# Performance work log

Hardware: AMD Instinct MI355X
Metric: run time of the kernel (lower is better)

The kernel has to match this reference:

```python
import jax, jax.numpy as jnp
import numpy as np


def _sepconv1x1(x, dw, pw, b):
    # SeparableConv2D with kernel=1: depthwise 1x1 = per-channel scale, then pointwise matmul
    return jnp.einsum('nhwc,cd->nhwd', x * dw, pw) + b


def setup_inputs() -> dict:
    key = jax.random.key(0)
    ks = jax.random.split(key, 12)
    N, H, W, C_in, C_red = 4, 64, 64, 256, 64
    s = 0.05  # small init so softmax logits are well-conditioned
    return {
        'feature_maps': jax.random.normal(ks[0], (N, H, W, C_in), jnp.float32),
        'global_channel_output': jax.random.normal(ks[1], (N, H, W, C_in), jnp.float32),
        'dw_q': jax.random.normal(ks[2], (C_in,), jnp.float32) * s,
        'pw_q': jax.random.normal(ks[3], (C_in, C_red), jnp.float32) * s,
        'b_q': jnp.zeros((C_red,), jnp.float32),
        'dw_k': jax.random.normal(ks[4], (C_in,), jnp.float32) * s,
        'pw_k': jax.random.normal(ks[5], (C_in, C_red), jnp.float32) * s,
        'b_k': jnp.zeros((C_red,), jnp.float32),
        'dw_v': jax.random.normal(ks[6], (C_in,), jnp.float32) * s,
        'pw_v': jax.random.normal(ks[7], (C_in, C_red), jnp.float32) * s,
        'b_v': jnp.zeros((C_red,), jnp.float32),
        'dw_a': jax.random.normal(ks[8], (C_red,), jnp.float32) * s,
        'pw_a': jax.random.normal(ks[9], (C_red, C_in), jnp.float32) * s,
        'b_a': jnp.zeros((C_in,), jnp.float32),
    }


def reference(feature_maps, global_channel_output,
              dw_q, pw_q, b_q, dw_k, pw_k, b_k, dw_v, pw_v, b_v,
              dw_a, pw_a, b_a):
    N, H, W, _ = feature_maps.shape
    q = _sepconv1x1(feature_maps, dw_q, pw_q, b_q)  # [N,H,W,Cr]
    k = _sepconv1x1(feature_maps, dw_k, pw_k, b_k)
    v = _sepconv1x1(feature_maps, dw_v, pw_v, b_v)
    Cr = q.shape[-1]
    q = q.reshape(N, H * W, Cr)
    k = k.reshape(N, H * W, Cr)
    v = v.reshape(N, H * W, Cr)
    # tf.matmul(key, query, transpose_b=True): scores[i,j] = key_i . query_j
    scores = jnp.einsum('nic,njc->nij', k, q)  # [N,HW,HW]
    scores = jax.nn.softmax(scores, axis=-1)
    # tf.matmul(value, scores, transpose_a=True) -> [N,Cr,HW]
    att = jnp.einsum('nic,nij->ncj', v, scores)
    # faithful raw reshape (as in the original TF code) from [N,Cr,HW] to [N,H,W,Cr]
    att = att.reshape(N, H, W, Cr)
    att = _sepconv1x1(att, dw_a, pw_a, b_a)  # [N,H,W,C_in]
    return global_channel_output * att + global_channel_output
```

## Files before the change

kernel.cpp:

```cpp
#include <hip/hip_runtime.h>
#include <hip/hip_bf16.h>

typedef __attribute__((ext_vector_type(8))) __bf16 bf16x8;
typedef __attribute__((ext_vector_type(4))) float floatx4;
typedef __attribute__((ext_vector_type(4))) unsigned short us4;
typedef __attribute__((ext_vector_type(8))) unsigned short us8;
typedef __attribute__((ext_vector_type(4))) short s16x4;
typedef __attribute__((ext_vector_type(2))) unsigned int uint2v;

#define MFMA16(A, B, C) __builtin_amdgcn_mfma_f32_16x16x32_bf16((A), (B), (C), 0, 0, 0)
#define MFMA1K(A, B, C) __builtin_amdgcn_mfma_f32_16x16x16bf16_1k((A), (B), (C), 0, 0, 0)

static __device__ __forceinline__ unsigned short f2bfbits(float f) {
    __hip_bfloat16 h = __float2bfloat16(f);
    union { __hip_bfloat16 h; unsigned short u; } cv;
    cv.h = h;
    return cv.u;
}
static __device__ __forceinline__ unsigned int rne32(float f) {
    unsigned int u = __builtin_bit_cast(unsigned int, f);
    return u + 0x7fffu + ((u >> 16) & 1u);
}
static __device__ __forceinline__ unsigned short rne16(float f) {
    return (unsigned short)(rne32(f) >> 16);
}
static __device__ __forceinline__ s16x4 pack4(float e0, float e1, float e2, float e3) {
    unsigned int pa = __builtin_amdgcn_perm(rne32(e1), rne32(e0), 0x07060302u);
    unsigned int pb = __builtin_amdgcn_perm(rne32(e3), rne32(e2), 0x07060302u);
    uint2v u = {pa, pb};
    return __builtin_bit_cast(s16x4, u);
}
static __device__ __forceinline__ bf16x8 load_bf8(const __hip_bfloat16* p) {
    return *reinterpret_cast<const bf16x8*>(p);
}
static __device__ __forceinline__ bf16x8 cvt8(floatx4 a, floatx4 b) {
    us8 u;
#pragma unroll
    for (int i = 0; i < 4; i++) { u[i] = rne16(a[i]); u[4 + i] = rne16(b[i]); }
    return __builtin_bit_cast(bf16x8, u);
}
static __device__ __forceinline__ float bf2f(unsigned short u) {
    unsigned int w = ((unsigned int)u) << 16;
    return __builtin_bit_cast(float, w);
}


__global__ __launch_bounds__(256) void prep_w(
    const float* __restrict__ dwq, const float* __restrict__ pwq,
    const float* __restrict__ dwk, const float* __restrict__ pwk,
    const float* __restrict__ dwv, const float* __restrict__ pwv,
    __hip_bfloat16* __restrict__ wT)
{
    int idx = blockIdx.x * 256 + threadIdx.x;
    int p = idx >> 14;
    int r = idx & 16383;
    int d = r >> 8, c = r & 255;
    const float* dw = (p == 0) ? dwq : ((p == 1) ? dwk : dwv);
    const float* pw = (p == 0) ? pwq : ((p == 1) ? pwk : pwv);
    wT[idx] = __float2bfloat16(dw[c] * pw[c * 64 + d]);
}

__global__ __launch_bounds__(256) void proj_qkv(
    const float* __restrict__ x,
    const __hip_bfloat16* __restrict__ wT,
    const float* __restrict__ bqp, const float* __restrict__ bkp,
    const float* __restrict__ bvp,
    __hip_bfloat16* __restrict__ qf, __hip_bfloat16* __restrict__ kf,
    __hip_bfloat16* __restrict__ vf)
{
    int wg = blockIdx.x * 4 + (threadIdx.x >> 6);
    int p = wg >> 10;
    int wid = wg & 1023;
    int lane = threadIdx.x & 63;
    int l15 = lane & 15, quad = lane >> 4;
    int strip = wid << 4;

    floatx4 acc[4];
#pragma unroll
    for (int t = 0; t < 4; t++) acc[t] = (floatx4){0.f, 0.f, 0.f, 0.f};

    const float* xrow = x + (strip + l15) * 256 + quad * 8;
    const __hip_bfloat16* wp = wT + p * 16384;
#pragma unroll
    for (int ks = 0; ks < 8; ks++) {
        floatx4 xa = *reinterpret_cast<const floatx4*>(xrow + ks * 32);
        floatx4 xb = *reinterpret_cast<const floatx4*>(xrow + ks * 32 + 4);
        bf16x8 a = cvt8(xa, xb);
#pragma unroll
        for (int t = 0; t < 4; t++) {
            bf16x8 b = load_bf8(wp + (t * 16 + l15) * 256 + ks * 32 + quad * 8);
            acc[t] = MFMA16(a, b, acc[t]);
        }
    }
    if (p < 2) {
        __hip_bfloat16* dst = (p == 0) ? qf : kf;
        const float* bias = (p == 0) ? bqp : bkp;
#pragma unroll
        for (int t = 0; t < 4; t++) {
            float bsv = bias[t * 16 + l15];
            int off0 = wid * 1024 + (t >> 1) * 512 +
                       (((((t & 1) << 1) | (l15 >> 3)) * 16 + quad * 4) * 8) + (l15 & 7);
#pragma unroll
            for (int r = 0; r < 4; r++)
                dst[off0 + r * 8] = __float2bfloat16(acc[t][r] + bsv);
        }
    } else {
#pragma unroll
        for (int t = 0; t < 4; t++) {
            float bsv = bvp[t * 16 + l15];
            us4 pk;
#pragma unroll
            for (int r = 0; r < 4; r++) pk[r] = f2bfbits(acc[t][r] + bsv);
            *reinterpret_cast<us4*>(vf + (wid * 4 + t) * 256 + lane * 4) = pk;
        }
    }
}

__global__ __launch_bounds__(512) void pass1_rl(
    const __hip_bfloat16* __restrict__ qf, const __hip_bfloat16* __restrict__ kf,
    const __hip_bfloat16* __restrict__ vf, __hip_bfloat16* __restrict__ vfs)
{
    int itg0 = blockIdx.x * 2;
    int n = itg0 >> 8;
    int jw = threadIdx.x >> 6;
    int lane = threadIdx.x & 63;
    int l15 = lane & 15, quad = lane >> 4;

    const __hip_bfloat16* kp = kf + itg0 * 1024 + lane * 8;
    bf16x8 a0 = load_bf8(kp);
    bf16x8 a1 = load_bf8(kp + 512);
    bf16x8 a2 = load_bf8(kp + 1024);
    bf16x8 a3 = load_bf8(kp + 1536);

    floatx4 lsA = (floatx4){0.f, 0.f, 0.f, 0.f};
    floatx4 lsB = (floatx4){0.f, 0.f, 0.f, 0.f};
    const __hip_bfloat16* qp0 = qf + (n * 256 + jw * 32) * 1024 + lane * 8;
    for (int it = 0; it < 16; it++, qp0 += 2048) {
        bf16x8 b0 = load_bf8(qp0);
        bf16x8 b1 = load_bf8(qp0 + 512);
        bf16x8 b2 = load_bf8(qp0 + 1024);
        bf16x8 b3 = load_bf8(qp0 + 1536);
        floatx4 z = (floatx4){0.f, 0.f, 0.f, 0.f};
        floatx4 sA0 = MFMA16(a1, b1, MFMA16(a0, b0, z));
        floatx4 sA1 = MFMA16(a1, b3, MFMA16(a0, b2, z));
        floatx4 sB0 = MFMA16(a3, b1, MFMA16(a2, b0, z));
        floatx4 sB1 = MFMA16(a3, b3, MFMA16(a2, b2, z));
#pragma unroll
        for (int r = 0; r < 4; r++) {
            lsA[r] += __expf(sA0[r]) + __expf(sA1[r]);
            lsB[r] += __expf(sB0[r]) + __expf(sB1[r]);
        }
    }
#pragma unroll
    for (int m = 1; m < 16; m <<= 1) {
#pragma unroll
        for (int r = 0; r < 4; r++) {
            lsA[r] += __shfl_xor(lsA[r], m, 64);
            lsB[r] += __shfl_xor(lsB[r], m, 64);
        }
    }
    __shared__ float red[8][32];
    __shared__ float rls[32];
    if (l15 == 0) {
#pragma unroll
        for (int r = 0; r < 4; r++) {
            red[jw][quad * 4 + r] = lsA[r];
            red[jw][16 + quad * 4 + r] = lsB[r];
        }
    }
    __syncthreads();
    if (threadIdx.x < 32) {
        float tot = 0.f;
#pragma unroll
        for (int w = 0; w < 8; w++) tot += red[w][threadIdx.x];
        rls[threadIdx.x] = 1.0f / tot;
    }
    __syncthreads();
    int m0 = threadIdx.x * 4;
    int toff = m0 >> 10;
    int mm = m0 & 1023;
    int rb = toff * 16 + ((mm >> 6) & 3) * 4;
    const unsigned short* vin = reinterpret_cast<const unsigned short*>(vf) + itg0 * 1024 + m0;
    us4 vv = *reinterpret_cast<const us4*>(vin);
    us4 ov;
#pragma unroll
    for (int r = 0; r < 4; r++) ov[r] = rne16(bf2f(vv[r]) * rls[rb + r]);
    *reinterpret_cast<us4*>(reinterpret_cast<unsigned short*>(vfs) + itg0 * 1024 + m0) = ov;
}

__global__ __launch_bounds__(256) void pass2_att(
    const __hip_bfloat16* __restrict__ qf, const __hip_bfloat16* __restrict__ kf,
    const __hip_bfloat16* __restrict__ vfs,
    unsigned short* __restrict__ attp)
{
    int b = blockIdx.x;
    int ih = b & 7;
    int g = b >> 3;
    int n = g >> 5;
    int jg = g & 31;
    int w = threadIdx.x >> 6;
    int jt0 = jg * 8 + w * 2;
    int lane = threadIdx.x & 63;
    int l15 = lane & 15, quad = lane >> 4;

    const __hip_bfloat16* qp = qf + (n * 256 + jt0) * 1024 + lane * 8;
    bf16x8 bq00 = load_bf8(qp);
    bf16x8 bq01 = load_bf8(qp + 512);
    bf16x8 bq10 = load_bf8(qp + 1024);
    bf16x8 bq11 = load_bf8(qp + 1536);

    floatx4 acc0[4], acc1[4];
#pragma unroll
    for (int t = 0; t < 4; t++) {
        acc0[t] = (floatx4){0.f, 0.f, 0.f, 0.f};
        acc1[t] = (floatx4){0.f, 0.f, 0.f, 0.f};
    }

    int it0 = n * 256 + ih * 32;
    const __hip_bfloat16* kp = kf + it0 * 1024 + lane * 8;
    const __hip_bfloat16* vp = vfs + it0 * 1024;
    for (int it = 0; it < 32; it++, kp += 1024, vp += 1024) {
        bf16x8 a0 = load_bf8(kp);
        bf16x8 a1 = load_bf8(kp + 512);
        floatx4 z = (floatx4){0.f, 0.f, 0.f, 0.f};
        floatx4 s0a = MFMA16(a0, bq00, z);
        floatx4 s0b = MFMA16(a1, bq01, z);
        floatx4 s1a = MFMA16(a0, bq10, z);
        floatx4 s1b = MFMA16(a1, bq11, z);
        floatx4 s0 = s0a + s0b;
        floatx4 s1 = s1a + s1b;
        s16x4 p0 = pack4(__expf(s0[0]), __expf(s0[1]), __expf(s0[2]), __expf(s0[3]));
        s16x4 p1 = pack4(__expf(s1[0]), __expf(s1[1]), __expf(s1[2]), __expf(s1[3]));
#pragma unroll
        for (int t = 0; t < 4; t++) {
            s16x4 bv = *reinterpret_cast<const s16x4*>(vp + t * 256 + lane * 4);
            acc0[t] = MFMA1K(p0, bv, acc0[t]);
            acc1[t] = MFMA1K(p1, bv, acc1[t]);
        }
    }
    unsigned short* op0 = attp + ih * 1048576;
#pragma unroll
    for (int t = 0; t < 4; t++) {
        s16x4 k0 = pack4(acc0[t][0], acc0[t][1], acc0[t][2], acc0[t][3]);
        s16x4 k1 = pack4(acc1[t][0], acc1[t][1], acc1[t][2], acc1[t][3]);
        unsigned short* op = op0 + (n * 64 + t * 16 + l15) * 4096 + jt0 * 16 + quad * 4;
        *reinterpret_cast<s16x4*>(op) = k0;
        *reinterpret_cast<s16x4*>(op + 16) = k1;
    }
}

__global__ __launch_bounds__(256) void final_out(
    const unsigned short* __restrict__ attp, const float* __restrict__ gco,
    const float* __restrict__ dwa, const float* __restrict__ pwa,
    const float* __restrict__ ba, float* __restrict__ out)
{
    int b = blockIdx.x;
    int n = b >> 9;
    int hh = (b >> 3) & 63;
    int w0 = (b & 7) << 3;
    __shared__ float g[512];
    int tid = threadIdx.x;
    const unsigned short* ap = attp + (n * 64 + hh) * 4096 + w0 * 64;
    for (int jj = tid; jj < 512; jj += 256) {
        float v = 0.f;
#pragma unroll
        for (int ph = 0; ph < 8; ph++) v += bf2f(ap[ph * 1048576 + jj]);
        g[jj] = v * dwa[jj & 63];
    }
    __syncthreads();
    float acc[8];
#pragma unroll
    for (int w = 0; w < 8; w++) acc[w] = 0.f;
    for (int cc = 0; cc < 64; cc++) {
        float p = pwa[cc * 256 + tid];
#pragma unroll
        for (int w = 0; w < 8; w++) acc[w] += g[w * 64 + cc] * p;
    }
    float bb = ba[tid];
#pragma unroll
    for (int w = 0; w < 8; w++) {
        int pos = (n * 64 + hh) * 64 + w0 + w;
        float gv = gco[pos * 256 + tid];
        out[pos * 256 + tid] = gv * (acc[w] + bb) + gv;
    }
}

extern "C" void kernel_launch(void* const* d_in, const int* in_sizes, int n_in,
                              void* d_out, int out_size, void* d_ws, size_t ws_size,
                              hipStream_t stream) {
    const float* x   = (const float*)d_in[0];
    const float* gco = (const float*)d_in[1];
    const float* dwq = (const float*)d_in[2];
    const float* pwq = (const float*)d_in[3];
    const float* bq  = (const float*)d_in[4];
    const float* dwk = (const float*)d_in[5];
    const float* pwk = (const float*)d_in[6];
    const float* bk  = (const float*)d_in[7];
    const float* dwv = (const float*)d_in[8];
    const float* pwv = (const float*)d_in[9];
    const float* bv  = (const float*)d_in[10];
    const float* dwa = (const float*)d_in[11];
    const float* pwa = (const float*)d_in[12];
    const float* ba  = (const float*)d_in[13];
    float* out = (float*)d_out;

    char* ws = (char*)d_ws;
    __hip_bfloat16* wT  = (__hip_bfloat16*)ws;
    __hip_bfloat16* qf  = (__hip_bfloat16*)(ws + 98304);
    __hip_bfloat16* kf  = (__hip_bfloat16*)(ws + 2195456);
    __hip_bfloat16* vf  = (__hip_bfloat16*)(ws + 4292608);
    __hip_bfloat16* vfs = (__hip_bfloat16*)(ws + 6389760);
    unsigned short* attp = (unsigned short*)(ws + 8486912);

    prep_w<<<192, 256, 0, stream>>>(dwq, pwq, dwk, pwk, dwv, pwv, wT);
    proj_qkv<<<768, 256, 0, stream>>>(x, wT, bq, bk, bv, qf, kf, vf);
    pass1_rl<<<512, 512, 0, stream>>>(qf, kf, vf, vfs);
    pass2_att<<<1024, 256, 0, stream>>>(qf, kf, vfs, attp);
    final_out<<<2048, 256, 0, stream>>>(attp, gco, dwa, pwa, ba, out);
}
```

Before: 182.6 us.

## Fold log2e into key weights, use raw v_exp, and split attention reduction further

Scales the key projection weights and bias by log2(e) so the softmax exponentials can use the hardware base-2 exp instruction directly through inline asm, removing the extra multiply that __expf adds. The attention pass is split into 16 partial sums over key rows instead of 8, doubling the grid for more parallelism, and the final kernel reduces 16 partials with paired vector loads. Packing of exponentials and accumulators to bf16 now truncates instead of rounding to nearest even. The trade-offs are a larger partial buffer and more reduction traffic in the final kernel, slightly lower precision from truncation, and a possible workspace overrun if the buffer was sized for 8 partials.

```diff
diff --git a/kernel.cpp b/kernel.cpp
--- a/kernel.cpp
+++ b/kernel.cpp
@@ -3,6 +3,7 @@
 
 typedef __attribute__((ext_vector_type(8))) __bf16 bf16x8;
 typedef __attribute__((ext_vector_type(4))) float floatx4;
+typedef __attribute__((ext_vector_type(2))) unsigned short us2;
 typedef __attribute__((ext_vector_type(4))) unsigned short us4;
 typedef __attribute__((ext_vector_type(8))) unsigned short us8;
 typedef __attribute__((ext_vector_type(4))) short s16x4;
@@ -10,6 +11,8 @@
 
 #define MFMA16(A, B, C) __builtin_amdgcn_mfma_f32_16x16x32_bf16((A), (B), (C), 0, 0, 0)
 #define MFMA1K(A, B, C) __builtin_amdgcn_mfma_f32_16x16x16bf16_1k((A), (B), (C), 0, 0, 0)
+
+#define LOG2E 1.44269504088896340736f
 
 static __device__ __forceinline__ unsigned short f2bfbits(float f) {
     __hip_bfloat16 h = __float2bfloat16(f);
@@ -24,24 +27,52 @@
 static __device__ __forceinline__ unsigned short rne16(float f) {
     return (unsigned short)(rne32(f) >> 16);
 }
-static __device__ __forceinline__ s16x4 pack4(float e0, float e1, float e2, float e3) {
-    unsigned int pa = __builtin_amdgcn_perm(rne32(e1), rne32(e0), 0x07060302u);
-    unsigned int pb = __builtin_amdgcn_perm(rne32(e3), rne32(e2), 0x07060302u);
-    uint2v u = {pa, pb};
-    return __builtin_bit_cast(s16x4, u);
+static __device__ __forceinline__ bf16x8 cvt8(floatx4 a, floatx4 b) {
+    us8 u;
+#pragma unroll
+    for (int i = 0; i < 4; i++) { u[i] = rne16(a[i]); u[4 + i] = rne16(b[i]); }
+    return __builtin_bit_cast(bf16x8, u);
 }
 static __device__ __forceinline__ bf16x8 load_bf8(const __hip_bfloat16* p) {
     return *reinterpret_cast<const bf16x8*>(p);
-}
-static __device__ __forceinline__ bf16x8 cvt8(floatx4 a, floatx4 b) {
-    us8 u;
-#pragma unroll
-    for (int i = 0; i < 4; i++) { u[i] = rne16(a[i]); u[4 + i] = rne16(b[i]); }
-    return __builtin_bit_cast(bf16x8, u);
 }
 static __device__ __forceinline__ float bf2f(unsigned short u) {
     unsigned int w = ((unsigned int)u) << 16;
     return __builtin_bit_cast(float, w);
+}
+
+static __device__ __forceinline__ s16x4 exp4_pack(float a0, float a1, float a2, float a3) {
+    float r0, r1, r2, r3;
+    unsigned int lo, hi;
+    asm("v_exp_f32 %0, %6\n\t"
+        "v_exp_f32 %1, %7\n\t"
+        "v_exp_f32 %2, %8\n\t"
+        "v_exp_f32 %3, %9\n\t"
+        "v_perm_b32 %4, %1, %0, %10\n\t"
+        "v_perm_b32 %5, %3, %2, %10"
+        : "=&v"(r0), "=&v"(r1), "=&v"(r2), "=&v"(r3), "=&v"(lo), "=v"(hi)
+        : "v"(a0), "v"(a1), "v"(a2), "v"(a3), "s"(0x07060302u));
+    uint2v u = {lo, hi};
+    return __builtin_bit_cast(s16x4, u);
+}
+static __device__ __forceinline__ float exp2_add(float a, float b) {
+    float r0, r1, s;
+    asm("v_exp_f32 %0, %3\n\t"
+        "v_exp_f32 %1, %4\n\t"
+        "s_nop 0\n\t"
+        "v_add_f32 %2, %0, %1"
+        : "=&v"(r0), "=&v"(r1), "=v"(s)
+        : "v"(a), "v"(b));
+    return s;
+}
+static __device__ __forceinline__ s16x4 pack4t(float e0, float e1, float e2, float e3) {
+    unsigned int b0 = __builtin_bit_cast(unsigned int, e0);
+    unsigned int b1 = __builtin_bit_cast(unsigned int, e1);
+    unsigned int b2 = __builtin_bit_cast(unsigned int, e2);
+    unsigned int b3 = __builtin_bit_cast(unsigned int, e3);
+    uint2v u = {__builtin_amdgcn_perm(b1, b0, 0x07060302u),
+                __builtin_amdgcn_perm(b3, b2, 0x07060302u)};
+    return __builtin_bit_cast(s16x4, u);
 }
 
 
@@ -57,7 +88,8 @@
     int d = r >> 8, c = r & 255;
     const float* dw = (p == 0) ? dwq : ((p == 1) ? dwk : dwv);
     const float* pw = (p == 0) ? pwq : ((p == 1) ? pwk : pwv);
-    wT[idx] = __float2bfloat16(dw[c] * pw[c * 64 + d]);
+    float scale = (p == 1) ? LOG2E : 1.0f;
+    wT[idx] = __float2bfloat16(dw[c] * pw[c * 64 + d] * scale);
 }
 
 __global__ __launch_bounds__(256) void proj_qkv(
@@ -95,9 +127,10 @@
     if (p < 2) {
         __hip_bfloat16* dst = (p == 0) ? qf : kf;
         const float* bias = (p == 0) ? bqp : bkp;
+        float bscale = (p == 1) ? LOG2E : 1.0f;
 #pragma unroll
         for (int t = 0; t < 4; t++) {
-            float bsv = bias[t * 16 + l15];
+            float bsv = bias[t * 16 + l15] * bscale;
             int off0 = wid * 1024 + (t >> 1) * 512 +
                        (((((t & 1) << 1) | (l15 >> 3)) * 16 + quad * 4) * 8) + (l15 & 7);
 #pragma unroll
@@ -147,8 +180,8 @@
         floatx4 sB1 = MFMA16(a3, b3, MFMA16(a2, b2, z));
 #pragma unroll
         for (int r = 0; r < 4; r++) {
-            lsA[r] += __expf(sA0[r]) + __expf(sA1[r]);
-            lsB[r] += __expf(sB0[r]) + __expf(sB1[r]);
+            lsA[r] += exp2_add(sA0[r], sA1[r]);
+            lsB[r] += exp2_add(sB0[r], sB1[r]);
         }
     }
 #pragma unroll
@@ -194,8 +227,8 @@
     unsigned short* __restrict__ attp)
 {
     int b = blockIdx.x;
-    int ih = b & 7;
-    int g = b >> 3;
+    int ih = b & 15;
+    int g = b >> 4;
     int n = g >> 5;
     int jg = g & 31;
     int w = threadIdx.x >> 6;
@@ -216,21 +249,17 @@
         acc1[t] = (floatx4){0.f, 0.f, 0.f, 0.f};
     }
 
-    int it0 = n * 256 + ih * 32;
+    int it0 = n * 256 + ih * 16;
     const __hip_bfloat16* kp = kf + it0 * 1024 + lane * 8;
     const __hip_bfloat16* vp = vfs + it0 * 1024;
-    for (int it = 0; it < 32; it++, kp += 1024, vp += 1024) {
+    for (int it = 0; it < 16; it++, kp += 1024, vp += 1024) {
         bf16x8 a0 = load_bf8(kp);
         bf16x8 a1 = load_bf8(kp + 512);
         floatx4 z = (floatx4){0.f, 0.f, 0.f, 0.f};
-        floatx4 s0a = MFMA16(a0, bq00, z);
-        floatx4 s0b = MFMA16(a1, bq01, z);
-        floatx4 s1a = MFMA16(a0, bq10, z);
-        floatx4 s1b = MFMA16(a1, bq11, z);
-        floatx4 s0 = s0a + s0b;
-        floatx4 s1 = s1a + s1b;
-        s16x4 p0 = pack4(__expf(s0[0]), __expf(s0[1]), __expf(s0[2]), __expf(s0[3]));
-        s16x4 p1 = pack4(__expf(s1[0]), __expf(s1[1]), __expf(s1[2]), __expf(s1[3]));
+        floatx4 s0 = MFMA16(a1, bq01, MFMA16(a0, bq00, z));
+        floatx4 s1 = MFMA16(a1, bq11, MFMA16(a0, bq10, z));
+        s16x4 p0 = exp4_pack(s0[0], s0[1], s0[2], s0[3]);
+        s16x4 p1 = exp4_pack(s1[0], s1[1], s1[2], s1[3]);
 #pragma unroll
         for (int t = 0; t < 4; t++) {
             s16x4 bv = *reinterpret_cast<const s16x4*>(vp + t * 256 + lane * 4);
@@ -241,8 +270,8 @@
     unsigned short* op0 = attp + ih * 1048576;
 #pragma unroll
     for (int t = 0; t < 4; t++) {
-        s16x4 k0 = pack4(acc0[t][0], acc0[t][1], acc0[t][2], acc0[t][3]);
-        s16x4 k1 = pack4(acc1[t][0], acc1[t][1], acc1[t][2], acc1[t][3]);
+        s16x4 k0 = pack4t(acc0[t][0], acc0[t][1], acc0[t][2], acc0[t][3]);
+        s16x4 k1 = pack4t(acc1[t][0], acc1[t][1], acc1[t][2], acc1[t][3]);
         unsigned short* op = op0 + (n * 64 + t * 16 + l15) * 4096 + jt0 * 16 + quad * 4;
         *reinterpret_cast<s16x4*>(op) = k0;
         *reinterpret_cast<s16x4*>(op + 16) = k1;
@@ -261,11 +290,16 @@
     __shared__ float g[512];
     int tid = threadIdx.x;
     const unsigned short* ap = attp + (n * 64 + hh) * 4096 + w0 * 64;
-    for (int jj = tid; jj < 512; jj += 256) {
-        float v = 0.f;
-#pragma unroll
-        for (int ph = 0; ph < 8; ph++) v += bf2f(ap[ph * 1048576 + jj]);
-        g[jj] = v * dwa[jj & 63];
+    {
+        float v0 = 0.f, v1 = 0.f;
+#pragma unroll
+        for (int ph = 0; ph < 16; ph++) {
+            us2 vv = *reinterpret_cast<const us2*>(ap + ph * 1048576 + tid * 2);
+            v0 += bf2f(vv[0]);
+            v1 += bf2f(vv[1]);
+        }
+        g[tid * 2]     = v0 * dwa[(tid * 2) & 63];
+        g[tid * 2 + 1] = v1 * dwa[(tid * 2 + 1) & 63];
     }
     __syncthreads();
     float acc[8];
@@ -315,6 +349,6 @@
     prep_w<<<192, 256, 0, stream>>>(dwq, pwq, dwk, pwk, dwv, pwv, wT);
     proj_qkv<<<768, 256, 0, stream>>>(x, wT, bq, bk, bv, qf, kf, vf);
     pass1_rl<<<512, 512, 0, stream>>>(qf, kf, vf, vfs);
-    pass2_att<<<1024, 256, 0, stream>>>(qf, kf, vfs, attp);
+    pass2_att<<<2048, 256, 0, stream>>>(qf, kf, vfs, attp);
     final_out<<<2048, 256, 0, stream>>>(attp, gco, dwa, pwa, ba, out);
 }
```

Result: slower. 205.2 us (+12.4%).
